# Optimization experiments

Measured on AMD Instinct MI355X. Metric: run time of the kernel, lower is better.

## Reference

```python
import jax, jax.numpy as jnp
import numpy as np

B, S, D, UNITS = 8, 2048, 512, 512

def setup_inputs() -> dict:
    key = jax.random.key(0)
    k1, k2, k3, k4 = jax.random.split(key, 4)
    scale = 1.0 / np.sqrt(D)
    return {
        "x": jax.random.normal(k1, (B, S, D), dtype=jnp.float32),
        "Wq": jax.random.normal(k2, (D, UNITS), dtype=jnp.float32) * scale,
        "Wk": jax.random.normal(k3, (D, UNITS), dtype=jnp.float32) * scale,
        "Wv": jax.random.normal(k4, (D, UNITS), dtype=jnp.float32) * scale,
    }

def reference(x, Wq, Wk, Wv):
    # Q, K, V: [B, S, units]
    Q = jnp.einsum('bsd,du->bsu', x, Wq)
    Km = jnp.einsum('bsd,du->bsu', x, Wk)
    V = jnp.einsum('bsd,du->bsu', x, Wv)
    d_k = jnp.asarray(Wq.shape[-1], dtype=x.dtype)
    # scores: [B, S, S]
    scores = jnp.einsum('bqu,bku->bqk', Q, Km) / jnp.sqrt(d_k)
    attn = jax.nn.softmax(scores, axis=-1)
    return jnp.einsum('bqk,bku->bqu', attn, V)
```

## Files before the change

kernel.cpp:

```cpp
#include <hip/hip_runtime.h>

typedef __attribute__((ext_vector_type(8))) __bf16 bf16x8;
typedef __attribute__((ext_vector_type(4))) float f32x4;
typedef unsigned short u16;
typedef unsigned int u32;

#define VMCNT(n) asm volatile("s_waitcnt vmcnt(" #n ")" ::: "memory")

__device__ __forceinline__ u16 f2bf(float f) {
  union { float f; u32 u; } v; v.f = f;
  u32 r = v.u + 0x7FFFu + ((v.u >> 16) & 1u);
  return (u16)(r >> 16);
}
__device__ __forceinline__ float fexp2(float x) {
  float r; asm("v_exp_f32 %0, %1" : "=v"(r) : "v"(x)); return r;
}

__global__ __launch_bounds__(256) void cast_x_kernel(const float* __restrict__ x,
                                                     u16* __restrict__ xb, int n4) {
  int i = blockIdx.x * 256 + threadIdx.x;
  if (i >= n4) return;
  float4 v = reinterpret_cast<const float4*>(x)[i];
  ushort4 o;
  o.x = f2bf(v.x); o.y = f2bf(v.y); o.z = f2bf(v.z); o.w = f2bf(v.w);
  reinterpret_cast<ushort4*>(xb)[i] = o;
}

__global__ __launch_bounds__(1024) void transpose_w_kernel(const float* __restrict__ Wq,
                                                           const float* __restrict__ Wk,
                                                           const float* __restrict__ Wv,
                                                           u16* __restrict__ Wt) {
  const float* src = blockIdx.z == 0 ? Wq : (blockIdx.z == 1 ? Wk : Wv);
  u16* dst = Wt + (size_t)blockIdx.z * 512 * 512;
  __shared__ float tile[32][33];
  int u0 = blockIdx.x * 32, d0 = blockIdx.y * 32;
  tile[threadIdx.y][threadIdx.x] = src[(d0 + threadIdx.y) * 512 + u0 + threadIdx.x];
  __syncthreads();
  dst[(u0 + threadIdx.y) * 512 + d0 + threadIdx.x] = f2bf(tile[threadIdx.x][threadIdx.y]);
}

__global__ __launch_bounds__(256) void qkv_kernel(const u16* __restrict__ Xb,
                                                  const u16* __restrict__ Wt3,
                                                  u16* __restrict__ Q, u16* __restrict__ K,
                                                  u16* __restrict__ Vt2) {
  __shared__ u16 As[3][128 * 32], Bs[3][128 * 32];
  const int bm = blockIdx.y * 128;
  const int bn = blockIdx.x * 128;
  const int z = blockIdx.z;
  const u16* A = Xb + (size_t)bm * 512;
  const u16* Bt = Wt3 + (size_t)z * 512 * 512 + (size_t)bn * 512;

  const int t = threadIdx.x;
  const int lane = t & 63;
  const int w = t >> 6;
  const int wr = w >> 1, wc = w & 1;
  const int la = lane & 15;
  const int q = lane >> 4;
  f32x4 acc[4][4] = {};

  auto stage = [&](int buf, int kt) {
    const int k0 = kt * 32;
#pragma unroll
    for (int it = 0; it < 2; ++it) {
      int c = it * 256 + t, row = c >> 2;
      int col = ((c & 3) ^ ((row >> 1) & 3)) << 3;
      __builtin_amdgcn_global_load_lds(
          (const __attribute__((address_space(1))) void*)(A + (size_t)row * 512 + k0 + col),
          (__attribute__((address_space(3))) void*)(&As[buf][c * 8]), 16, 0, 0);
    }
#pragma unroll
    for (int it = 0; it < 2; ++it) {
      int c = it * 256 + t, row = c >> 2;
      int col = ((c & 3) ^ ((row >> 1) & 3)) << 3;
      __builtin_amdgcn_global_load_lds(
          (const __attribute__((address_space(1))) void*)(Bt + (size_t)row * 512 + k0 + col),
          (__attribute__((address_space(3))) void*)(&Bs[buf][c * 8]), 16, 0, 0);
    }
  };

  auto body = [&](int buf) {
    bf16x8 a[4], b[4];
#pragma unroll
    for (int i = 0; i < 4; ++i) {
      int row = wr * 64 + i * 16 + la;
      a[i] = *reinterpret_cast<const bf16x8*>(&As[buf][row * 32 + ((q ^ ((row >> 1) & 3)) << 3)]);
    }
#pragma unroll
    for (int j = 0; j < 4; ++j) {
      int row = wc * 64 + j * 16 + la;
      b[j] = *reinterpret_cast<const bf16x8*>(&Bs[buf][row * 32 + ((q ^ ((row >> 1) & 3)) << 3)]);
    }
    __builtin_amdgcn_s_setprio(1);
#pragma unroll
    for (int i = 0; i < 4; ++i)
#pragma unroll
      for (int j = 0; j < 4; ++j)
        acc[i][j] = __builtin_amdgcn_mfma_f32_16x16x32_bf16(a[i], b[j], acc[i][j], 0, 0, 0);
    __builtin_amdgcn_s_setprio(0);
  };

  stage(0, 0); stage(1, 1);
  int cb = 0, sb = 2;
  for (int kt = 0; kt < 14; ++kt) {
    VMCNT(4);
    __builtin_amdgcn_s_barrier();
    stage(sb, kt + 2);
    body(cb);
    cb = (cb == 2) ? 0 : cb + 1;
    sb = (sb == 2) ? 0 : sb + 1;
  }
  VMCNT(4); __builtin_amdgcn_s_barrier(); body(2);
  VMCNT(0); __builtin_amdgcn_s_barrier(); body(0);

  const int r0 = q * 4, cn = lane & 15;
  if (z < 2) {
    u16* out = (z == 0) ? Q : K;
#pragma unroll
    for (int i = 0; i < 4; ++i)
#pragma unroll
      for (int j = 0; j < 4; ++j)
#pragma unroll
        for (int r = 0; r < 4; ++r) {
          int m = bm + 64 * wr + 16 * i + r0 + r;
          int n = bn + 64 * wc + 16 * j + cn;
          out[(size_t)m * 512 + n] = f2bf(acc[i][j][r]);
        }
  } else {
#pragma unroll
    for (int i = 0; i < 4; ++i)
#pragma unroll
      for (int j = 0; j < 4; ++j)
#pragma unroll
        for (int r = 0; r < 4; ++r) {
          int m = bm + 64 * wr + 16 * i + r0 + r;
          int u = bn + 64 * wc + 16 * j + cn;
          int b = m >> 11, s = m & 2047;
          Vt2[(((size_t)b * 64 + (s >> 5)) * 512 + u) * 32 + (s & 31)] = f2bf(acc[i][j][r]);
        }
  }
}

__global__ __launch_bounds__(512) void scores8_kernel(const u16* __restrict__ Q,
                                                      const u16* __restrict__ K,
                                                      u16* __restrict__ S2) {
  __shared__ u16 ring[4][2][256 * 32];
  const int bb = blockIdx.x;
  const int bm = blockIdx.y * 256;
  const int bn = blockIdx.z * 256;
  const u16* Aq = Q + (size_t)(bb * 2048 + bm) * 512;
  const u16* Bk = K + (size_t)(bb * 2048 + bn) * 512;

  const int t = threadIdx.x;
  const int lane = t & 63;
  const int wid = t >> 6;
  const int wm = wid >> 2, wn = wid & 3;
  const int la = lane & 15;
  const int q = lane >> 4;

  f32x4 acc[8][4] = {};

  auto stage = [&](int kt) {
    const int r = kt & 3;
    const int koff = kt * 32;
#pragma unroll
    for (int half = 0; half < 2; ++half) {
      int c = half * 512 + t;
      int row = c >> 2;
      int col = ((c & 3) ^ ((row >> 1) & 3)) << 3;
      __builtin_amdgcn_global_load_lds(
          (const __attribute__((address_space(1))) void*)(Aq + (size_t)row * 512 + koff + col),
          (__attribute__((address_space(3))) void*)(&ring[r][0][c * 8]), 16, 0, 0);
      __builtin_amdgcn_global_load_lds(
          (const __attribute__((address_space(1))) void*)(Bk + (size_t)row * 512 + koff + col),
          (__attribute__((address_space(3))) void*)(&ring[r][1][c * 8]), 16, 0, 0);
    }
  };

  auto body = [&](int kt) {
    const int r = kt & 3;
    const u16* At = ring[r][0];
    const u16* Bt = ring[r][1];
    bf16x8 bfr[4], afr[8];
#pragma unroll
    for (int j = 0; j < 4; ++j) {
      int row = wn * 64 + j * 16 + la;
      bfr[j] = *reinterpret_cast<const bf16x8*>(Bt + row * 32 + ((q ^ ((row >> 1) & 3)) << 3));
    }
#pragma unroll
    for (int i = 0; i < 8; ++i) {
      int row = wm * 128 + i * 16 + la;
      afr[i] = *reinterpret_cast<const bf16x8*>(At + row * 32 + ((q ^ ((row >> 1) & 3)) << 3));
    }
    __builtin_amdgcn_s_setprio(1);
#pragma unroll
    for (int i = 0; i < 8; ++i)
#pragma unroll
      for (int j = 0; j < 4; ++j)
        acc[i][j] = __builtin_amdgcn_mfma_f32_16x16x32_bf16(afr[i], bfr[j], acc[i][j], 0, 0, 0);
    __builtin_amdgcn_s_setprio(0);
  };

  stage(0); stage(1); stage(2);
  for (int kt = 0; kt < 13; ++kt) {
    VMCNT(8);
    __builtin_amdgcn_s_barrier();
    stage(kt + 3);
    body(kt);
  }
  VMCNT(8); __builtin_amdgcn_s_barrier(); body(13);
  VMCNT(4); __builtin_amdgcn_s_barrier(); body(14);
  VMCNT(0); __builtin_amdgcn_s_barrier(); body(15);

  const float scale = 0.06375872127f;
  const int r0h = q * 4;
#pragma unroll
  for (int i = 0; i < 8; ++i)
#pragma unroll
    for (int j = 0; j < 4; ++j) {
      int n = bn + wn * 64 + j * 16;
      int kt_j = n >> 5;
      int ke_j = (n & 31) + la;
      u16* dst = S2 + ((size_t)(bb * 64 + kt_j) * 2048) * 32 + ke_j;
#pragma unroll
      for (int r = 0; r < 4; ++r) {
        int m = bm + wm * 128 + i * 16 + r0h + r;
        dst[(size_t)m * 32] = f2bf(fexp2(acc[i][j][r] * scale));
      }
    }
}

__global__ __launch_bounds__(512) void pv_kernel(const u16* __restrict__ S2,
                                                 const u16* __restrict__ Vt2,
                                                 float* __restrict__ out) {
  __shared__ u16 As[3][2][256 * 32];
  __shared__ u16 Bs[3][2][128 * 32];
  __shared__ float larr[256];
  const int id = blockIdx.x;
  const int b = id & 7;
  const int local = id >> 3;
  const int bn = (local & 3) * 128;
  const int bm = (local >> 2) * 256;

  const u16* A2 = S2 + ((size_t)b * 64 * 2048 + (size_t)bm) * 32;
  const u16* B2 = Vt2 + ((size_t)b * 64 * 512 + (size_t)bn) * 32;

  const int t = threadIdx.x;
  const int lane = t & 63;
  const int wid = t >> 6;
  const int wm = wid >> 1;
  const int wn = wid & 1;
  const int la = lane & 15;
  const int q = lane >> 4;

  f32x4 acc[4][4] = {};
  float lacc[4] = {0.f, 0.f, 0.f, 0.f};

  auto stage = [&](int s) {
    const int buf = s % 3;
#pragma unroll
    for (int it = 0; it < 4; ++it) {
      int c = it * 512 + t;
      int h = c >> 10;
      int idx = c & 1023;
      int row = idx >> 2;
      int col = ((c & 3) ^ ((row >> 1) & 3)) << 3;
      __builtin_amdgcn_global_load_lds(
          (const __attribute__((address_space(1))) void*)(A2 + (size_t)(2 * s + h) * 65536 + row * 32 + col),
          (__attribute__((address_space(3))) void*)(&As[buf][0][c * 8]), 16, 0, 0);
    }
#pragma unroll
    for (int it = 0; it < 2; ++it) {
      int c = it * 512 + t;
      int h = c >> 9;
      int idx = c & 511;
      int row = idx >> 2;
      int col = ((c & 3) ^ ((row >> 1) & 3)) << 3;
      __builtin_amdgcn_global_load_lds(
          (const __attribute__((address_space(1))) void*)(B2 + (size_t)(2 * s + h) * 16384 + row * 32 + col),
          (__attribute__((address_space(3))) void*)(&Bs[buf][0][c * 8]), 16, 0, 0);
    }
  };

  auto body = [&](int s) {
    const int buf = s % 3;
#pragma unroll
    for (int h = 0; h < 2; ++h) {
      const u16* Ah = &As[buf][h][0];
      const u16* Bh = &Bs[buf][h][0];
      bf16x8 a[4], bb[4];
#pragma unroll
      for (int i = 0; i < 4; ++i) {
        int row = wm * 64 + i * 16 + la;
        a[i] = *reinterpret_cast<const bf16x8*>(Ah + row * 32 + ((q ^ ((row >> 1) & 3)) << 3));
      }
      if (wn == 0) {
#pragma unroll
        for (int i = 0; i < 4; ++i) {
          float ls = 0.f;
#pragma unroll
          for (int e = 0; e < 8; ++e) ls += (float)a[i][e];
          lacc[i] += ls;
        }
      }
#pragma unroll
      for (int j = 0; j < 4; ++j) {
        int row = wn * 64 + j * 16 + la;
        bb[j] = *reinterpret_cast<const bf16x8*>(Bh + row * 32 + ((q ^ ((row >> 1) & 3)) << 3));
      }
      __builtin_amdgcn_s_setprio(1);
#pragma unroll
      for (int i = 0; i < 4; ++i)
#pragma unroll
        for (int j = 0; j < 4; ++j)
          acc[i][j] = __builtin_amdgcn_mfma_f32_16x16x32_bf16(a[i], bb[j], acc[i][j], 0, 0, 0);
      __builtin_amdgcn_s_setprio(0);
    }
  };

  stage(0); stage(1);
  for (int s = 0; s < 30; ++s) {
    VMCNT(6);
    __builtin_amdgcn_s_barrier();
    stage(s + 2);
    body(s);
  }
  VMCNT(6); __builtin_amdgcn_s_barrier(); body(30);
  VMCNT(0); __builtin_amdgcn_s_barrier(); body(31);

  float l[4];
#pragma unroll
  for (int i = 0; i < 4; ++i) {
    l[i] = lacc[i];
    l[i] += __shfl_xor(l[i], 16);
    l[i] += __shfl_xor(l[i], 32);
  }
  if (wn == 0 && q == 0) {
#pragma unroll
    for (int i = 0; i < 4; ++i) larr[wm * 64 + i * 16 + la] = l[i];
  }
  __syncthreads();

  float* C = out + ((size_t)b * 2048 + bm) * 512;
  const int r0 = q * 4, cn = lane & 15;
  float inv[4][4];
#pragma unroll
  for (int i = 0; i < 4; ++i)
#pragma unroll
    for (int r = 0; r < 4; ++r)
      inv[i][r] = 1.0f / larr[wm * 64 + i * 16 + r0 + r];
#pragma unroll
  for (int i = 0; i < 4; ++i)
#pragma unroll
    for (int j = 0; j < 4; ++j)
#pragma unroll
      for (int r = 0; r < 4; ++r) {
        int m = wm * 64 + 16 * i + r0 + r;
        int n = bn + 64 * wn + 16 * j + cn;
        C[(size_t)m * 512 + n] = acc[i][j][r] * inv[i][r];
      }
}

extern "C" void kernel_launch(void* const* d_in, const int* in_sizes, int n_in,
                              void* d_out, int out_size, void* d_ws, size_t ws_size,
                              hipStream_t stream) {
  const float* x  = (const float*)d_in[0];
  const float* Wq = (const float*)d_in[1];
  const float* Wk = (const float*)d_in[2];
  const float* Wv = (const float*)d_in[3];
  float* out = (float*)d_out;

  char* p = (char*)d_ws;
  u16* Xb = (u16*)p;            p += (size_t)16384 * 512 * 2;
  u16* Wt = (u16*)p;            p += (size_t)3 * 512 * 512 * 2;
  u16* Q  = (u16*)p;            p += (size_t)16384 * 512 * 2;
  u16* K  = (u16*)p;            p += (size_t)16384 * 512 * 2;
  u16* Vt2 = (u16*)p;           p += (size_t)16384 * 512 * 2;
  u16* S2 = (u16*)p;

  cast_x_kernel<<<dim3(8192), dim3(256), 0, stream>>>(x, Xb, 16384 * 512 / 4);
  transpose_w_kernel<<<dim3(16, 16, 3), dim3(32, 32), 0, stream>>>(Wq, Wk, Wv, Wt);
  qkv_kernel<<<dim3(4, 128, 3), dim3(256), 0, stream>>>(Xb, Wt, Q, K, Vt2);
  scores8_kernel<<<dim3(8, 8, 8), dim3(512), 0, stream>>>(Q, K, S2);
  pv_kernel<<<dim3(256), dim3(512), 0, stream>>>(S2, Vt2, out);
}
```

Measured before the change: 152.3 us.

## Interleave LDS reads, async stages and MFMA quadrants in PV GEMM loop

Restructures the main loop of the attention-times-V GEMM so that each stage is split into four MFMA quadrants. Fragment reads from LDS and the individual global-to-LDS prefetch loads are interleaved between them, separated by barriers in a ping-pong style schedule. The intent is to overlap LDS reads and memory issue with matrix-core work instead of doing all loads and then all MFMAs. It adds many more barriers per iteration and keeps more fragment registers live, which could reduce overlap across waves or raise register pressure.

Measured after the change: 148.1 us. -2.8%, faster.

```diff
diff --git a/kernel.cpp b/kernel.cpp
--- a/kernel.cpp
+++ b/kernel.cpp
@@ -254,78 +254,135 @@
 
   f32x4 acc[4][4] = {};
   float lacc[4] = {0.f, 0.f, 0.f, 0.f};
-
-  auto stage = [&](int s) {
+  bf16x8 a[4][2], bfr[4][2];
+
+  auto stageA = [&](int s, int it) {
     const int buf = s % 3;
-#pragma unroll
-    for (int it = 0; it < 4; ++it) {
-      int c = it * 512 + t;
-      int h = c >> 10;
-      int idx = c & 1023;
-      int row = idx >> 2;
-      int col = ((c & 3) ^ ((row >> 1) & 3)) << 3;
-      __builtin_amdgcn_global_load_lds(
-          (const __attribute__((address_space(1))) void*)(A2 + (size_t)(2 * s + h) * 65536 + row * 32 + col),
-          (__attribute__((address_space(3))) void*)(&As[buf][0][c * 8]), 16, 0, 0);
-    }
-#pragma unroll
-    for (int it = 0; it < 2; ++it) {
-      int c = it * 512 + t;
-      int h = c >> 9;
-      int idx = c & 511;
-      int row = idx >> 2;
-      int col = ((c & 3) ^ ((row >> 1) & 3)) << 3;
-      __builtin_amdgcn_global_load_lds(
-          (const __attribute__((address_space(1))) void*)(B2 + (size_t)(2 * s + h) * 16384 + row * 32 + col),
-          (__attribute__((address_space(3))) void*)(&Bs[buf][0][c * 8]), 16, 0, 0);
-    }
-  };
-
-  auto body = [&](int s) {
+    int c = it * 512 + t;
+    int h = c >> 10;
+    int idx = c & 1023;
+    int row = idx >> 2;
+    int col = ((c & 3) ^ ((row >> 1) & 3)) << 3;
+    __builtin_amdgcn_global_load_lds(
+        (const __attribute__((address_space(1))) void*)(A2 + (size_t)(2 * s + h) * 65536 + row * 32 + col),
+        (__attribute__((address_space(3))) void*)(&As[buf][0][c * 8]), 16, 0, 0);
+  };
+  auto stageB = [&](int s, int it) {
     const int buf = s % 3;
+    int c = it * 512 + t;
+    int h = c >> 9;
+    int idx = c & 511;
+    int row = idx >> 2;
+    int col = ((c & 3) ^ ((row >> 1) & 3)) << 3;
+    __builtin_amdgcn_global_load_lds(
+        (const __attribute__((address_space(1))) void*)(B2 + (size_t)(2 * s + h) * 16384 + row * 32 + col),
+        (__attribute__((address_space(3))) void*)(&Bs[buf][0][c * 8]), 16, 0, 0);
+  };
+  auto stage6 = [&](int s) {
+    stageA(s, 0); stageA(s, 1); stageA(s, 2); stageA(s, 3);
+    stageB(s, 0); stageB(s, 1);
+  };
+
+  auto rdA = [&](int buf, int i) {
 #pragma unroll
     for (int h = 0; h < 2; ++h) {
-      const u16* Ah = &As[buf][h][0];
-      const u16* Bh = &Bs[buf][h][0];
-      bf16x8 a[4], bb[4];
-#pragma unroll
-      for (int i = 0; i < 4; ++i) {
-        int row = wm * 64 + i * 16 + la;
-        a[i] = *reinterpret_cast<const bf16x8*>(Ah + row * 32 + ((q ^ ((row >> 1) & 3)) << 3));
+      int row = wm * 64 + i * 16 + la;
+      a[i][h] = *reinterpret_cast<const bf16x8*>(&As[buf][h][row * 32 + ((q ^ ((row >> 1) & 3)) << 3)]);
+    }
+  };
+  auto rdB = [&](int buf, int j) {
+#pragma unroll
+    for (int h = 0; h < 2; ++h) {
+      int row = wn * 64 + j * 16 + la;
+      bfr[j][h] = *reinterpret_cast<const bf16x8*>(&Bs[buf][h][row * 32 + ((q ^ ((row >> 1) & 3)) << 3)]);
+    }
+  };
+  auto mm = [&](int i0, int j0) {
+    __builtin_amdgcn_s_setprio(1);
+#pragma unroll
+    for (int i = 0; i < 2; ++i)
+#pragma unroll
+      for (int j = 0; j < 2; ++j)
+#pragma unroll
+        for (int h = 0; h < 2; ++h)
+          acc[i0 + i][j0 + j] =
+              __builtin_amdgcn_mfma_f32_16x16x32_bf16(a[i0 + i][h], bfr[j0 + j][h], acc[i0 + i][j0 + j], 0, 0, 0);
+    __builtin_amdgcn_s_setprio(0);
+  };
+  auto lsum = [&](int i0) {
+    if (wn == 0) {
+#pragma unroll
+      for (int i = 0; i < 2; ++i) {
+        float ls = 0.f;
+#pragma unroll
+        for (int h = 0; h < 2; ++h)
+#pragma unroll
+          for (int e = 0; e < 8; ++e) ls += (float)a[i0 + i][h][e];
+        lacc[i0 + i] += ls;
       }
-      if (wn == 0) {
-#pragma unroll
-        for (int i = 0; i < 4; ++i) {
-          float ls = 0.f;
-#pragma unroll
-          for (int e = 0; e < 8; ++e) ls += (float)a[i][e];
-          lacc[i] += ls;
-        }
-      }
-#pragma unroll
-      for (int j = 0; j < 4; ++j) {
-        int row = wn * 64 + j * 16 + la;
-        bb[j] = *reinterpret_cast<const bf16x8*>(Bh + row * 32 + ((q ^ ((row >> 1) & 3)) << 3));
-      }
-      __builtin_amdgcn_s_setprio(1);
-#pragma unroll
-      for (int i = 0; i < 4; ++i)
-#pragma unroll
-        for (int j = 0; j < 4; ++j)
-          acc[i][j] = __builtin_amdgcn_mfma_f32_16x16x32_bf16(a[i], bb[j], acc[i][j], 0, 0, 0);
-      __builtin_amdgcn_s_setprio(0);
-    }
-  };
-
-  stage(0); stage(1);
+    }
+  };
+
+  stage6(0); stage6(1);
+  VMCNT(6); __builtin_amdgcn_s_barrier();
   for (int s = 0; s < 30; ++s) {
+    const int buf = s % 3;
+    rdA(buf, 0); rdA(buf, 1); rdB(buf, 0); rdB(buf, 1);
+    stageA(s + 2, 0); stageB(s + 2, 0);
+    __builtin_amdgcn_s_barrier();
+    mm(0, 0); lsum(0);
+    __builtin_amdgcn_s_barrier();
+    rdB(buf, 2); rdB(buf, 3);
+    stageA(s + 2, 1); stageB(s + 2, 1);
+    __builtin_amdgcn_s_barrier();
+    mm(0, 2);
+    __builtin_amdgcn_s_barrier();
+    rdA(buf, 2); rdA(buf, 3);
+    stageA(s + 2, 2);
+    __builtin_amdgcn_s_barrier();
+    mm(2, 0); lsum(2);
+    __builtin_amdgcn_s_barrier();
+    stageA(s + 2, 3);
     VMCNT(6);
     __builtin_amdgcn_s_barrier();
-    stage(s + 2);
-    body(s);
-  }
-  VMCNT(6); __builtin_amdgcn_s_barrier(); body(30);
-  VMCNT(0); __builtin_amdgcn_s_barrier(); body(31);
+    mm(2, 2);
+    __builtin_amdgcn_s_barrier();
+  }
+  {
+    const int buf = 0;
+    rdA(buf, 0); rdA(buf, 1); rdB(buf, 0); rdB(buf, 1);
+    __builtin_amdgcn_s_barrier();
+    mm(0, 0); lsum(0);
+    __builtin_amdgcn_s_barrier();
+    rdB(buf, 2); rdB(buf, 3);
+    __builtin_amdgcn_s_barrier();
+    mm(0, 2);
+    __builtin_amdgcn_s_barrier();
+    rdA(buf, 2); rdA(buf, 3);
+    __builtin_amdgcn_s_barrier();
+    mm(2, 0); lsum(2);
+    __builtin_amdgcn_s_barrier();
+    VMCNT(0);
+    __builtin_amdgcn_s_barrier();
+    mm(2, 2);
+    __builtin_amdgcn_s_barrier();
+  }
+  {
+    const int buf = 1;
+    rdA(buf, 0); rdA(buf, 1); rdB(buf, 0); rdB(buf, 1);
+    __builtin_amdgcn_s_barrier();
+    mm(0, 0); lsum(0);
+    __builtin_amdgcn_s_barrier();
+    rdB(buf, 2); rdB(buf, 3);
+    __builtin_amdgcn_s_barrier();
+    mm(0, 2);
+    __builtin_amdgcn_s_barrier();
+    rdA(buf, 2); rdA(buf, 3);
+    __builtin_amdgcn_s_barrier();
+    mm(2, 0); lsum(2);
+    __builtin_amdgcn_s_barrier();
+    mm(2, 2);
+  }
 
   float l[4];
 #pragma unroll
```

## Split PV kernel K-dimension across warps and halve M tile for more blocks

Applied to the files above, without the earlier changes.

The PV GEMM tile shrinks from 256x128 to 128x128 and the grid grows from 256 to 512 blocks, so the work fills more of the chip's compute units. Within each block, the 8 warps now split the K dimension in two (wk), each reading half of a 64-wide k-slab. The partial results are reduced through shared memory before normalisation. Buffering drops from triple to double with a new XOR swizzle, and LDS reads are separated from compute by an extra barrier. The cost is an extra reduction pass, an additional sync per iteration, and shallower prefetching.

Result: faster. 140.2 us (-7.9%).

```diff
diff --git a/kernel.cpp b/kernel.cpp
--- a/kernel.cpp
+++ b/kernel.cpp
@@ -6,6 +6,7 @@
 typedef unsigned int u32;
 
 #define VMCNT(n) asm volatile("s_waitcnt vmcnt(" #n ")" ::: "memory")
+#define LGKMCNT0 asm volatile("s_waitcnt lgkmcnt(0)" ::: "memory")
 
 __device__ __forceinline__ u16 f2bf(float f) {
   union { float f; u32 u; } v; v.f = f;
@@ -229,17 +230,20 @@
     }
 }
 
-__global__ __launch_bounds__(512) void pv_kernel(const u16* __restrict__ S2,
-                                                 const u16* __restrict__ Vt2,
-                                                 float* __restrict__ out) {
-  __shared__ u16 As[3][2][256 * 32];
-  __shared__ u16 Bs[3][2][128 * 32];
-  __shared__ float larr[256];
+__global__ __launch_bounds__(512, 4) void pv_kernel(const u16* __restrict__ S2,
+                                                    const u16* __restrict__ Vt2,
+                                                    float* __restrict__ out) {
+  __shared__ __align__(16) char smem[65536];
+  __shared__ float larr2[2][128];
+  u16* As = (u16*)smem;
+  u16* Bs = As + 2 * 8192;
+  float* scratch = (float*)smem;
+
   const int id = blockIdx.x;
   const int b = id & 7;
   const int local = id >> 3;
   const int bn = (local & 3) * 128;
-  const int bm = (local >> 2) * 256;
+  const int bm = (local >> 2) * 128;
 
   const u16* A2 = S2 + ((size_t)b * 64 * 2048 + (size_t)bm) * 32;
   const u16* B2 = Vt2 + ((size_t)b * 64 * 512 + (size_t)bn) * 32;
@@ -247,8 +251,9 @@
   const int t = threadIdx.x;
   const int lane = t & 63;
   const int wid = t >> 6;
-  const int wm = wid >> 1;
-  const int wn = wid & 1;
+  const int wm = (wid >> 2) & 1;
+  const int wn = (wid >> 1) & 1;
+  const int wk = wid & 1;
   const int la = lane & 15;
   const int q = lane >> 4;
 
@@ -256,76 +261,80 @@
   float lacc[4] = {0.f, 0.f, 0.f, 0.f};
 
   auto stage = [&](int s) {
-    const int buf = s % 3;
-#pragma unroll
-    for (int it = 0; it < 4; ++it) {
-      int c = it * 512 + t;
-      int h = c >> 10;
-      int idx = c & 1023;
-      int row = idx >> 2;
-      int col = ((c & 3) ^ ((row >> 1) & 3)) << 3;
-      __builtin_amdgcn_global_load_lds(
-          (const __attribute__((address_space(1))) void*)(A2 + (size_t)(2 * s + h) * 65536 + row * 32 + col),
-          (__attribute__((address_space(3))) void*)(&As[buf][0][c * 8]), 16, 0, 0);
-    }
+    const int buf = s & 1;
 #pragma unroll
     for (int it = 0; it < 2; ++it) {
       int c = it * 512 + t;
-      int h = c >> 9;
-      int idx = c & 511;
-      int row = idx >> 2;
-      int col = ((c & 3) ^ ((row >> 1) & 3)) << 3;
-      __builtin_amdgcn_global_load_lds(
-          (const __attribute__((address_space(1))) void*)(B2 + (size_t)(2 * s + h) * 16384 + row * 32 + col),
-          (__attribute__((address_space(3))) void*)(&Bs[buf][0][c * 8]), 16, 0, 0);
-    }
-  };
-
-  auto body = [&](int s) {
-    const int buf = s % 3;
-#pragma unroll
-    for (int h = 0; h < 2; ++h) {
-      const u16* Ah = &As[buf][h][0];
-      const u16* Bh = &Bs[buf][h][0];
-      bf16x8 a[4], bb[4];
+      int row = c >> 3, pslot = c & 7;
+      int lslot = pslot ^ (row & 7);
+      __builtin_amdgcn_global_load_lds(
+          (const __attribute__((address_space(1))) void*)(
+              A2 + (size_t)(2 * s + (lslot >> 2)) * 65536 + row * 32 + (lslot & 3) * 8),
+          (__attribute__((address_space(3))) void*)(As + buf * 8192 + c * 8), 16, 0, 0);
+    }
+#pragma unroll
+    for (int it = 0; it < 2; ++it) {
+      int c = it * 512 + t;
+      int row = c >> 3, pslot = c & 7;
+      int lslot = pslot ^ (row & 7);
+      __builtin_amdgcn_global_load_lds(
+          (const __attribute__((address_space(1))) void*)(
+              B2 + (size_t)(2 * s + (lslot >> 2)) * 16384 + row * 32 + (lslot & 3) * 8),
+          (__attribute__((address_space(3))) void*)(Bs + buf * 8192 + c * 8), 16, 0, 0);
+    }
+  };
+
+  bf16x8 a[4], bb[4];
+  auto rd = [&](int buf) {
+    const u16* Ab = As + buf * 8192;
+    const u16* Bb = Bs + buf * 8192;
+#pragma unroll
+    for (int i = 0; i < 4; ++i) {
+      int row = wm * 64 + i * 16 + la;
+      int ps = (wk * 4 + q) ^ (row & 7);
+      a[i] = *reinterpret_cast<const bf16x8*>(Ab + row * 64 + ps * 8);
+    }
+#pragma unroll
+    for (int j = 0; j < 4; ++j) {
+      int row = wn * 64 + j * 16 + la;
+      int ps = (wk * 4 + q) ^ (row & 7);
+      bb[j] = *reinterpret_cast<const bf16x8*>(Bb + row * 64 + ps * 8);
+    }
+  };
+  auto compute = [&]() {
+    if (wn == 0) {
 #pragma unroll
       for (int i = 0; i < 4; ++i) {
-        int row = wm * 64 + i * 16 + la;
-        a[i] = *reinterpret_cast<const bf16x8*>(Ah + row * 32 + ((q ^ ((row >> 1) & 3)) << 3));
+        float ls = 0.f;
+#pragma unroll
+        for (int e = 0; e < 8; ++e) ls += (float)a[i][e];
+        lacc[i] += ls;
       }
-      if (wn == 0) {
-#pragma unroll
-        for (int i = 0; i < 4; ++i) {
-          float ls = 0.f;
-#pragma unroll
-          for (int e = 0; e < 8; ++e) ls += (float)a[i][e];
-          lacc[i] += ls;
-        }
-      }
-#pragma unroll
-      for (int j = 0; j < 4; ++j) {
-        int row = wn * 64 + j * 16 + la;
-        bb[j] = *reinterpret_cast<const bf16x8*>(Bh + row * 32 + ((q ^ ((row >> 1) & 3)) << 3));
-      }
-      __builtin_amdgcn_s_setprio(1);
-#pragma unroll
-      for (int i = 0; i < 4; ++i)
-#pragma unroll
-        for (int j = 0; j < 4; ++j)
-          acc[i][j] = __builtin_amdgcn_mfma_f32_16x16x32_bf16(a[i], bb[j], acc[i][j], 0, 0, 0);
-      __builtin_amdgcn_s_setprio(0);
-    }
+    }
+    __builtin_amdgcn_s_setprio(1);
+#pragma unroll
+    for (int i = 0; i < 4; ++i)
+#pragma unroll
+      for (int j = 0; j < 4; ++j)
+        acc[i][j] = __builtin_amdgcn_mfma_f32_16x16x32_bf16(a[i], bb[j], acc[i][j], 0, 0, 0);
+    __builtin_amdgcn_s_setprio(0);
   };
 
   stage(0); stage(1);
   for (int s = 0; s < 30; ++s) {
-    VMCNT(6);
+    VMCNT(4);
+    __builtin_amdgcn_s_barrier();
+    rd(s & 1);
+    LGKMCNT0;
     __builtin_amdgcn_s_barrier();
     stage(s + 2);
-    body(s);
-  }
-  VMCNT(6); __builtin_amdgcn_s_barrier(); body(30);
-  VMCNT(0); __builtin_amdgcn_s_barrier(); body(31);
+    compute();
+  }
+  VMCNT(4); __builtin_amdgcn_s_barrier();
+  rd(0); LGKMCNT0; __builtin_amdgcn_s_barrier(); compute();
+  VMCNT(0); __builtin_amdgcn_s_barrier();
+  rd(1); LGKMCNT0; __builtin_amdgcn_s_barrier();
+  compute();
 
   float l[4];
 #pragma unroll
@@ -336,28 +345,47 @@
   }
   if (wn == 0 && q == 0) {
 #pragma unroll
-    for (int i = 0; i < 4; ++i) larr[wm * 64 + i * 16 + la] = l[i];
+    for (int i = 0; i < 4; ++i) larr2[wk][wm * 64 + i * 16 + la] = l[i];
+  }
+  float* sp = scratch + (wid >> 1) * 4096;
+  if (wk == 1) {
+#pragma unroll
+    for (int i = 0; i < 4; ++i)
+#pragma unroll
+      for (int j = 0; j < 4; ++j)
+        *reinterpret_cast<f32x4*>(sp + (i * 4 + j) * 256 + lane * 4) = acc[i][j];
   }
   __syncthreads();
-
-  float* C = out + ((size_t)b * 2048 + bm) * 512;
-  const int r0 = q * 4, cn = lane & 15;
-  float inv[4][4];
-#pragma unroll
-  for (int i = 0; i < 4; ++i)
-#pragma unroll
-    for (int r = 0; r < 4; ++r)
-      inv[i][r] = 1.0f / larr[wm * 64 + i * 16 + r0 + r];
-#pragma unroll
-  for (int i = 0; i < 4; ++i)
-#pragma unroll
-    for (int j = 0; j < 4; ++j)
+  if (wk == 0) {
+#pragma unroll
+    for (int i = 0; i < 4; ++i)
+#pragma unroll
+      for (int j = 0; j < 4; ++j) {
+        f32x4 o = *reinterpret_cast<const f32x4*>(sp + (i * 4 + j) * 256 + lane * 4);
+#pragma unroll
+        for (int r = 0; r < 4; ++r) acc[i][j][r] += o[r];
+      }
+    float* C = out + ((size_t)b * 2048 + bm) * 512;
+    const int r0 = q * 4, cn = lane & 15;
+    float inv[4][4];
+#pragma unroll
+    for (int i = 0; i < 4; ++i)
 #pragma unroll
       for (int r = 0; r < 4; ++r) {
-        int m = wm * 64 + 16 * i + r0 + r;
-        int n = bn + 64 * wn + 16 * j + cn;
-        C[(size_t)m * 512 + n] = acc[i][j][r] * inv[i][r];
+        int row = wm * 64 + i * 16 + r0 + r;
+        inv[i][r] = 1.0f / (larr2[0][row] + larr2[1][row]);
       }
+#pragma unroll
+    for (int i = 0; i < 4; ++i)
+#pragma unroll
+      for (int j = 0; j < 4; ++j)
+#pragma unroll
+        for (int r = 0; r < 4; ++r) {
+          int m = wm * 64 + 16 * i + r0 + r;
+          int n = bn + 64 * wn + 16 * j + cn;
+          C[(size_t)m * 512 + n] = acc[i][j][r] * inv[i][r];
+        }
+  }
 }
 
 extern "C" void kernel_launch(void* const* d_in, const int* in_sizes, int n_in,
@@ -381,5 +409,5 @@
   transpose_w_kernel<<<dim3(16, 16, 3), dim3(32, 32), 0, stream>>>(Wq, Wk, Wv, Wt);
   qkv_kernel<<<dim3(4, 128, 3), dim3(256), 0, stream>>>(Xb, Wt, Q, K, Vt2);
   scores8_kernel<<<dim3(8, 8, 8), dim3(512), 0, stream>>>(Q, K, S2);
-  pv_kernel<<<dim3(256), dim3(512), 0, stream>>>(S2, Vt2, out);
-}
+  pv_kernel<<<dim3(512), dim3(512), 0, stream>>>(S2, Vt2, out);
+}
```
